# Kernel optimization log

Hardware: AMD Instinct MI355X
Metric: run time of the kernel (lower is better)

The kernel has to match this reference:

```python
import jax, jax.numpy as jnp
import numpy as np

C, R, T = 16, 1024, 4096
N = 500_000


def setup_inputs() -> dict:
    key = jax.random.key(0)
    k1, k2, k3 = jax.random.split(key, 3)
    rho = jax.random.randint(k1, (N,), 0, R, dtype=jnp.int32)
    theta = jax.random.randint(k2, (N,), 0, T, dtype=jnp.int32)
    f = jax.random.randint(k3, (N,), 0, C, dtype=jnp.int32)
    # buffers registered in __init__
    rp = jnp.arange(R + 1, dtype=jnp.float32)  # (R+1,)
    r = jnp.arange(R, dtype=jnp.float32)       # (R,)
    return {"rho": rho, "theta": theta, "f": f, "rp": rp, "r": r}


def reference(rho, theta, f, rp, r):
    # occ[f, rho, theta] = rho ; value stored equals its R-index, duplicates benign
    occ = jnp.full((C, R, T), -1, dtype=jnp.int32).at[f, rho, theta].set(rho)
    ids = jnp.argmax(occ, axis=1, keepdims=True)              # (C,1,T) largest occupied rho
    empty = jnp.all(occ == -1, axis=1, keepdims=True)         # no occupied point in column
    # torch uses ids=-1 -> rp[-1] == rp[R]; emulate wrap explicitly
    ids = jnp.where(empty, R, ids)
    return rp[ids] - r.reshape(1, -1, 1)                      # (C,R,T) float32
```

## Files before the change

kernel.cpp:

```cpp
#include <hip/hip_runtime.h>

#define C_DIM 16
#define R_DIM 1024
#define T_DIM 4096


__global__ void scatter_max(const int* __restrict__ rho,
                            const int* __restrict__ theta,
                            const int* __restrict__ f,
                            int* __restrict__ maxrho, int n) {
    int i = blockIdx.x * blockDim.x + threadIdx.x;
    if (i < n) {
        atomicMax(&maxrho[f[i] * T_DIM + theta[i]], rho[i]);
    }
}

__global__ void resolve(int* __restrict__ slot,
                        const float* __restrict__ rp) {
    int i = blockIdx.x * blockDim.x + threadIdx.x;
    int m = slot[i];
    float v = rp[m < 0 ? R_DIM : m];
    reinterpret_cast<float*>(slot)[i] = v;
}

__global__ void write_out(const float* __restrict__ val,
                          const float* __restrict__ r,
                          float* __restrict__ out) {
    int row = blockIdx.x;
    int rr  = row & (R_DIM - 1);
    int c   = row >> 10;
    float rv = r[rr];

    const float4* vrow = reinterpret_cast<const float4*>(val + c * T_DIM);
    float4* orow = reinterpret_cast<float4*>(out) + (size_t)row * (T_DIM / 4);

#pragma unroll
    for (int k = 0; k < 4; ++k) {
        int t4 = threadIdx.x + k * 256;
        float4 v = vrow[t4];
        float4 o = { v.x - rv, v.y - rv, v.z - rv, v.w - rv };
        orow[t4] = o;
    }
}

extern "C" void kernel_launch(void* const* d_in, const int* in_sizes, int n_in,
                              void* d_out, int out_size, void* d_ws, size_t ws_size,
                              hipStream_t stream) {
    const int*   rho   = (const int*)d_in[0];
    const int*   theta = (const int*)d_in[1];
    const int*   f     = (const int*)d_in[2];
    const float* rp    = (const float*)d_in[3];
    const float* r     = (const float*)d_in[4];
    float* out = (float*)d_out;

    int* slot = (int*)d_ws;
    const int n = in_sizes[0];

    hipMemsetAsync(slot, 0xFF, (size_t)C_DIM * T_DIM * sizeof(int), stream);

    scatter_max<<<(n + 255) / 256, 256, 0, stream>>>(rho, theta, f, slot, n);

    resolve<<<(C_DIM * T_DIM) / 256, 256, 0, stream>>>(slot, rp);

    write_out<<<C_DIM * R_DIM, 256, 0, stream>>>((const float*)slot, r, out);
}
```

Baseline: 73.26 us.

## Fuse resolve into write_out and emit multiple rows per block

Removes the separate resolve kernel and does the rp gather inside write_out. Each block now loads one channel's maxrho row once, resolves it into registers, and writes 16 output rows from them. This saves a kernel launch and the round trip through the workspace, and cuts redundant loads of the value row. The trade-off is far fewer blocks (1024 instead of 16384), with each block producing a much larger amount of store traffic.

```diff
diff --git a/kernel.cpp b/kernel.cpp
--- a/kernel.cpp
+++ b/kernel.cpp
@@ -3,6 +3,7 @@
 #define C_DIM 16
 #define R_DIM 1024
 #define T_DIM 4096
+#define ROWS_PER_BLOCK 16
 
 
 __global__ void scatter_max(const int* __restrict__ rho,
@@ -15,31 +16,36 @@
     }
 }
 
-__global__ void resolve(int* __restrict__ slot,
-                        const float* __restrict__ rp) {
-    int i = blockIdx.x * blockDim.x + threadIdx.x;
-    int m = slot[i];
-    float v = rp[m < 0 ? R_DIM : m];
-    reinterpret_cast<float*>(slot)[i] = v;
-}
+__global__ __launch_bounds__(256) void write_out(const int* __restrict__ maxrho,
+                                                 const float* __restrict__ rp,
+                                                 const float* __restrict__ r,
+                                                 float* __restrict__ out) {
+    const int c     = blockIdx.x >> 6;
+    const int chunk = blockIdx.x & 63;
+    const int rr0   = chunk * ROWS_PER_BLOCK;
 
-__global__ void write_out(const float* __restrict__ val,
-                          const float* __restrict__ r,
-                          float* __restrict__ out) {
-    int row = blockIdx.x;
-    int rr  = row & (R_DIM - 1);
-    int c   = row >> 10;
-    float rv = r[rr];
-
-    const float4* vrow = reinterpret_cast<const float4*>(val + c * T_DIM);
-    float4* orow = reinterpret_cast<float4*>(out) + (size_t)row * (T_DIM / 4);
-
+    const int4* mrow = reinterpret_cast<const int4*>(maxrho + c * T_DIM);
+    float v[16];
 #pragma unroll
     for (int k = 0; k < 4; ++k) {
-        int t4 = threadIdx.x + k * 256;
-        float4 v = vrow[t4];
-        float4 o = { v.x - rv, v.y - rv, v.z - rv, v.w - rv };
-        orow[t4] = o;
+        int4 m = mrow[threadIdx.x + k * 256];
+        v[4 * k + 0] = rp[m.x < 0 ? R_DIM : m.x];
+        v[4 * k + 1] = rp[m.y < 0 ? R_DIM : m.y];
+        v[4 * k + 2] = rp[m.z < 0 ? R_DIM : m.z];
+        v[4 * k + 3] = rp[m.w < 0 ? R_DIM : m.w];
+    }
+
+    float* obase = out + ((size_t)c * R_DIM + rr0) * T_DIM;
+
+    for (int j = 0; j < ROWS_PER_BLOCK; ++j) {
+        float rv = r[rr0 + j];
+        float4* orow = reinterpret_cast<float4*>(obase + (size_t)j * T_DIM);
+#pragma unroll
+        for (int k = 0; k < 4; ++k) {
+            float4 o = { v[4 * k + 0] - rv, v[4 * k + 1] - rv,
+                         v[4 * k + 2] - rv, v[4 * k + 3] - rv };
+            orow[threadIdx.x + k * 256] = o;
+        }
     }
 }
 
@@ -53,14 +59,12 @@
     const float* r     = (const float*)d_in[4];
     float* out = (float*)d_out;
 
-    int* slot = (int*)d_ws;
+    int* maxrho = (int*)d_ws;
     const int n = in_sizes[0];
 
-    hipMemsetAsync(slot, 0xFF, (size_t)C_DIM * T_DIM * sizeof(int), stream);
+    hipMemsetAsync(maxrho, 0xFF, (size_t)C_DIM * T_DIM * sizeof(int), stream);
 
-    scatter_max<<<(n + 255) / 256, 256, 0, stream>>>(rho, theta, f, slot, n);
+    scatter_max<<<(n + 255) / 256, 256, 0, stream>>>(rho, theta, f, maxrho, n);
 
-    resolve<<<(C_DIM * T_DIM) / 256, 256, 0, stream>>>(slot, rp);
-
-    write_out<<<C_DIM * R_DIM, 256, 0, stream>>>((const float*)slot, r, out);
+    write_out<<<C_DIM * (R_DIM / ROWS_PER_BLOCK), 256, 0, stream>>>(maxrho, rp, r, out);
 }
```

After: 113.7 us. 55.2% more time.
